# Kernel tuning notes

Hardware: AMD Instinct MI355X
Metric: run time of the kernel (lower is better)

## Reference

```python
import jax, jax.numpy as jnp
import numpy as np

N_POINTS = 1048576  # batch of evaluation points
HIDDEN = 128
N_HIDDEN_LAYERS = 9  # 128->128 layers between the input and output projections


def setup_inputs() -> dict:
    key = jax.random.key(0)
    ks = jax.random.split(key, 7)
    # Kaiming-ish scale so activations stay O(1) through the deep ReLU stack
    s_in = (2.0 / 4) ** 0.5
    s_h = (2.0 / HIDDEN) ** 0.5
    return {
        "x": jax.random.normal(ks[0], (N_POINTS, 4), dtype=jnp.float32),
        "W0": jax.random.normal(ks[1], (HIDDEN, 4), dtype=jnp.float32) * s_in,
        "b0": jnp.zeros((HIDDEN,), dtype=jnp.float32),
        "Wh": jax.random.normal(ks[2], (N_HIDDEN_LAYERS, HIDDEN, HIDDEN), dtype=jnp.float32) * s_h,
        "bh": jnp.zeros((N_HIDDEN_LAYERS, HIDDEN), dtype=jnp.float32),
        "Wout": jax.random.normal(ks[3], (1, HIDDEN), dtype=jnp.float32) * s_h,
        "bout": jnp.zeros((1,), dtype=jnp.float32),
    }


def reference(x, W0, b0, Wh, bh, Wout, bout):
    # Flatten: x is already [N, 4]; nn.Flatten collapses trailing dims to 4.
    h = jax.nn.relu(jnp.einsum("nd,hd->nh", x, W0) + b0)  # [N, 128]
    # 9 hidden Linear(128,128)+ReLU layers; small fixed layer loop (structural)
    for i in range(N_HIDDEN_LAYERS):
        h = jax.nn.relu(jnp.einsum("nh,oh->no", h, Wh[i]) + bh[i])
    logits = jnp.einsum("nh,oh->no", h, Wout) + bout  # [N, 1], no final ReLU
    return logits
```

## Files before the change

kernel.cpp:

```cpp
#include <hip/hip_runtime.h>
#include <stdint.h>

typedef _Float16 f16x8 __attribute__((ext_vector_type(8)));
typedef __fp16   fp16x2 __attribute__((ext_vector_type(2)));
typedef float    f32x16 __attribute__((ext_vector_type(16)));

union Frag {
  f16x8    v;
  uint32_t w[4];
  _Float16 h[8];
};

union CVec {
  float4 q[4];
  f32x16 v;
};

__device__ __forceinline__ uint32_t pack2h(float a, float b) {
  union { _Float16 h[2]; uint32_t u; } r;
  r.h[0] = (_Float16)a;
  r.h[1] = (_Float16)b;
  return r.u;
}

__device__ __forceinline__ uint32_t pkrtz(float a, float b) {
  union { fp16x2 h2; uint32_t u; } cv;
  cv.h2 = __builtin_amdgcn_cvt_pkrtz(a, b);
  return cv.u;
}

__device__ __forceinline__ void g2lds16(const void* g, void* l) {
  __builtin_amdgcn_global_load_lds(
      (const __attribute__((address_space(1))) uint32_t*)g,
      (__attribute__((address_space(3))) uint32_t*)l, 16, 0, 0);
}

__global__ void prep_kernel(const float* __restrict__ W0, const float* __restrict__ b0,
                            const float* __restrict__ Wh, const float* __restrict__ bh,
                            const float* __restrict__ Wout,
                            _Float16* __restrict__ wfrag, _Float16* __restrict__ w0frag,
                            float* __restrict__ biasC, _Float16* __restrict__ woutf16) {
  const int stride = gridDim.x * blockDim.x;
  for (int idx = blockIdx.x * blockDim.x + threadIdx.x; idx < 154880; idx += stride) {
    if (idx < 147456) {
      const int j = idx & 7, lane = (idx >> 3) & 63, kt = (idx >> 9) & 7,
                ot = (idx >> 12) & 3, l = idx >> 14;
      const int o = ot * 32 + (lane & 31);
      const int k = kt * 16 + (lane >> 5) * 8 + j;
      wfrag[idx] = (_Float16)Wh[(l * 128 + o) * 128 + k];
    } else if (idx < 147456 + 2048) {
      const int i = idx - 147456;
      const int j = i & 7, lane = (i >> 3) & 63, ot = i >> 9;
      const int o = ot * 32 + (lane & 31);
      const int k = (lane >> 5) * 8 + j;
      w0frag[i] = (_Float16)(k < 4 ? W0[o * 4 + k] : 0.0f);
    } else if (idx < 147456 + 2048 + 1280) {
      const int i = idx - (147456 + 2048);
      const int r = i & 15, hh = (i >> 4) & 1, ot = (i >> 5) & 3, l = i >> 7;
      const int row = (r & 3) + 8 * (r >> 2) + 4 * hh;
      const int o = ot * 32 + row;
      biasC[i] = (l == 0) ? b0[o] : bh[(l - 1) * 128 + o];
    } else {
      const int i = idx - (147456 + 2048 + 1280);
      const int j = i & 7, lane = (i >> 3) & 63, kt = i >> 9;
      const int k = kt * 16 + (lane >> 5) * 8 + j;
      woutf16[i] = ((lane & 31) == 0) ? (_Float16)Wout[k] : (_Float16)0.0f;
    }
  }
}

__global__ __launch_bounds__(256, 2) void mlp_fused(
    const float* __restrict__ x,
    const _Float16* __restrict__ wfrag,
    const _Float16* __restrict__ w0frag,
    const float* __restrict__ biasCg,
    const _Float16* __restrict__ woutf16,
    const float* __restrict__ boutp,
    float* __restrict__ out) {
  __shared__ __align__(16) unsigned char ldsW[2][32768];
  __shared__ __align__(16) float ldsBiasC[1280];

  const int t    = threadIdx.x;
  const int lane = t & 63;
  const int wv   = t >> 6;
  const int h    = lane >> 5;
  const int ln   = lane & 31;
  const long rowbase = (long)blockIdx.x * 256 + wv * 64;

  {
    const unsigned char* src = (const unsigned char*)wfrag;
#pragma unroll
    for (int i = 0; i < 8; ++i) {
      const int off = i * 4096 + t * 16;
      g2lds16(src + off, &ldsW[0][off]);
    }
    const unsigned char* bsrc = (const unsigned char*)biasCg;
    g2lds16(bsrc + t * 16, (unsigned char*)ldsBiasC + t * 16);
    if (t < 64) g2lds16(bsrc + (256 + t) * 16, (unsigned char*)ldsBiasC + (256 + t) * 16);
  }

  Frag   B[2][8];
  f32x16 acc[4][2];
  const f32x16 fzero = (f32x16)0.0f;

  auto load_cvec = [&](int l, int ot) -> f32x16 {
    CVec cv;
    const float* p = ldsBiasC + ((l * 4 + ot) * 2 + h) * 16;
#pragma unroll
    for (int g = 0; g < 4; ++g) cv.q[g] = *(const float4*)(p + g * 4);
    return cv.v;
  };

  Frag xb[2];
#pragma unroll
  for (int nt = 0; nt < 2; ++nt) {
    float4 xv = make_float4(0.f, 0.f, 0.f, 0.f);
    if (h == 0) xv = *(const float4*)(x + (rowbase + nt * 32 + ln) * 4);
    xb[nt].w[0] = pack2h(xv.x, xv.y);
    xb[nt].w[1] = pack2h(xv.z, xv.w);
    xb[nt].w[2] = 0u;
    xb[nt].w[3] = 0u;
  }

  __syncthreads();

#pragma unroll
  for (int ot = 0; ot < 4; ++ot) {
    const f16x8 a0 = *(const f16x8*)(w0frag + ot * 512 + lane * 8);
    const f32x16 cvec = load_cvec(0, ot);
    acc[ot][0] = __builtin_amdgcn_mfma_f32_32x32x16_f16(a0, xb[0].v, cvec, 0, 0, 0);
    acc[ot][1] = __builtin_amdgcn_mfma_f32_32x32x16_f16(a0, xb[1].v, cvec, 0, 0, 0);
  }

  auto do_epilogue = [&]() {
#pragma unroll
    for (int ot = 0; ot < 4; ++ot) {
#pragma unroll
      for (int nt = 0; nt < 2; ++nt) {
        uint32_t P[4][2];
#pragma unroll
        for (int g = 0; g < 4; ++g) {
#pragma unroll
          for (int c = 0; c < 2; ++c) {
            const uint32_t cv = pkrtz(acc[ot][nt][g * 4 + c * 2 + 0],
                                      acc[ot][nt][g * 4 + c * 2 + 1]);
            uint32_t r;
            asm("v_pk_max_f16 %0, %1, %2" : "=v"(r) : "v"(cv), "v"(0u));
            P[g][c] = r;
          }
        }
#pragma unroll
        for (int u = 0; u < 2; ++u) {
          uint32_t a0 = P[2 * u][0], b0v = P[2 * u + 1][0];
          uint32_t a1 = P[2 * u][1], b1v = P[2 * u + 1][1];
          asm("v_permlane32_swap_b32 %0, %1" : "+v"(a0), "+v"(b0v));
          asm("v_permlane32_swap_b32 %0, %1" : "+v"(a1), "+v"(b1v));
          Frag nb;
          nb.w[0] = a0;
          nb.w[1] = a1;
          nb.w[2] = b0v;
          nb.w[3] = b1v;
          B[nt][ot * 2 + u] = nb;
        }
      }
    }
  };

#pragma unroll
  for (int l = 1; l <= 9; ++l) {
    if (l < 9) {
      const unsigned char* src = (const unsigned char*)wfrag + (size_t)l * 32768;
#pragma unroll
      for (int i = 0; i < 8; ++i) {
        const int off = i * 4096 + t * 16;
        g2lds16(src + off, &ldsW[l & 1][off]);
      }
    }
    do_epilogue();
    const unsigned char* wl = &ldsW[(l - 1) & 1][0];
    __builtin_amdgcn_s_setprio(1);
#pragma unroll
    for (int kt = 0; kt < 8; ++kt) {
#pragma unroll
      for (int ot = 0; ot < 4; ++ot) {
        const f16x8 a = *(const f16x8*)(wl + ot * 8192 + kt * 1024 + lane * 16);
        if (kt == 0) {
          const f32x16 cvec = load_cvec(l, ot);
          acc[ot][0] = __builtin_amdgcn_mfma_f32_32x32x16_f16(a, B[0][kt].v, cvec, 0, 0, 0);
          acc[ot][1] = __builtin_amdgcn_mfma_f32_32x32x16_f16(a, B[1][kt].v, cvec, 0, 0, 0);
        } else {
          acc[ot][0] = __builtin_amdgcn_mfma_f32_32x32x16_f16(a, B[0][kt].v, acc[ot][0], 0, 0, 0);
          acc[ot][1] = __builtin_amdgcn_mfma_f32_32x32x16_f16(a, B[1][kt].v, acc[ot][1], 0, 0, 0);
        }
      }
    }
    __builtin_amdgcn_s_setprio(0);
    if (l < 9) __syncthreads();
  }

  {
    Frag wa[8];
#pragma unroll
    for (int kt = 0; kt < 8; ++kt)
      wa[kt].v = *(const f16x8*)(woutf16 + kt * 512 + lane * 8);
    const float boutv = *boutp;

    do_epilogue();

    f32x16 accO0 = fzero, accO1 = fzero;
#pragma unroll
    for (int kt = 0; kt < 8; ++kt) {
      accO0 = __builtin_amdgcn_mfma_f32_32x32x16_f16(wa[kt].v, B[0][kt].v, accO0, 0, 0, 0);
      accO1 = __builtin_amdgcn_mfma_f32_32x32x16_f16(wa[kt].v, B[1][kt].v, accO1, 0, 0, 0);
    }
    if (h == 0) {
      out[rowbase + ln]      = accO0[0] + boutv;
      out[rowbase + 32 + ln] = accO1[0] + boutv;
    }
  }
}

extern "C" void kernel_launch(void* const* d_in, const int* in_sizes, int n_in,
                              void* d_out, int out_size, void* d_ws, size_t ws_size,
                              hipStream_t stream) {
  (void)n_in; (void)out_size; (void)ws_size;
  const float* x    = (const float*)d_in[0];
  const float* W0   = (const float*)d_in[1];
  const float* b0   = (const float*)d_in[2];
  const float* Wh   = (const float*)d_in[3];
  const float* bh   = (const float*)d_in[4];
  const float* Wout = (const float*)d_in[5];
  const float* bout = (const float*)d_in[6];
  float* out = (float*)d_out;

  char* ws = (char*)d_ws;
  _Float16* wfrag   = (_Float16*)(ws);
  _Float16* w0frag  = (_Float16*)(ws + 294912);
  float*    biasC   = (float*)(ws + 299008);
  _Float16* woutf16 = (_Float16*)(ws + 304128);

  const int n = in_sizes[0] / 4;

  prep_kernel<<<dim3(160), dim3(256), 0, stream>>>(W0, b0, Wh, bh, Wout,
                                                   wfrag, w0frag, biasC, woutf16);
  mlp_fused<<<dim3(n / 256), dim3(256), 0, stream>>>(x, wfrag, w0frag, biasC,
                                                     woutf16, bout, out);
}
```

Measured before the change: 257.0 us.

## Halve rows per wave and double block threads to raise occupancy

Each wave now processes 32 rows instead of 64, and blocks grow to 512 threads covering the same 256 rows. Accumulator and activation-fragment registers per wave are halved, which allows more resident waves to hide the latency of the epilogue and MFMA chains. The cost is that each weight fragment loaded from LDS now feeds one MFMA instead of two, doubling LDS read traffic per row. Weight and bias staging loops are redistributed across the larger thread count.

```diff
diff --git a/kernel.cpp b/kernel.cpp
--- a/kernel.cpp
+++ b/kernel.cpp
@@ -69,7 +69,7 @@
   }
 }
 
-__global__ __launch_bounds__(256, 2) void mlp_fused(
+__global__ __launch_bounds__(512, 4) void mlp_fused(
     const float* __restrict__ x,
     const _Float16* __restrict__ wfrag,
     const _Float16* __restrict__ w0frag,
@@ -85,22 +85,23 @@
   const int wv   = t >> 6;
   const int h    = lane >> 5;
   const int ln   = lane & 31;
-  const long rowbase = (long)blockIdx.x * 256 + wv * 64;
+  const long rowbase = (long)blockIdx.x * 256 + wv * 32;
 
   {
     const unsigned char* src = (const unsigned char*)wfrag;
 #pragma unroll
-    for (int i = 0; i < 8; ++i) {
-      const int off = i * 4096 + t * 16;
+    for (int i = 0; i < 4; ++i) {
+      const int off = i * 8192 + t * 16;
       g2lds16(src + off, &ldsW[0][off]);
     }
-    const unsigned char* bsrc = (const unsigned char*)biasCg;
-    g2lds16(bsrc + t * 16, (unsigned char*)ldsBiasC + t * 16);
-    if (t < 64) g2lds16(bsrc + (256 + t) * 16, (unsigned char*)ldsBiasC + (256 + t) * 16);
-  }
-
-  Frag   B[2][8];
-  f32x16 acc[4][2];
+    if (t < 320) {
+      const unsigned char* bsrc = (const unsigned char*)biasCg;
+      g2lds16(bsrc + t * 16, (unsigned char*)ldsBiasC + t * 16);
+    }
+  }
+
+  Frag   B[8];
+  f32x16 acc[4];
   const f32x16 fzero = (f32x16)0.0f;
 
   auto load_cvec = [&](int l, int ot) -> f32x16 {
@@ -111,15 +112,42 @@
     return cv.v;
   };
 
-  Frag xb[2];
-#pragma unroll
-  for (int nt = 0; nt < 2; ++nt) {
+  auto e_chunk = [&](int ot) {
+    uint32_t P[4][2];
+#pragma unroll
+    for (int g = 0; g < 4; ++g) {
+#pragma unroll
+      for (int c = 0; c < 2; ++c) {
+        const uint32_t cv = pkrtz(acc[ot][g * 4 + c * 2 + 0],
+                                  acc[ot][g * 4 + c * 2 + 1]);
+        uint32_t r;
+        asm("v_pk_max_f16 %0, %1, %2" : "=v"(r) : "v"(cv), "v"(0u));
+        P[g][c] = r;
+      }
+    }
+#pragma unroll
+    for (int u = 0; u < 2; ++u) {
+      uint32_t a0 = P[2 * u][0], b0v = P[2 * u + 1][0];
+      uint32_t a1 = P[2 * u][1], b1v = P[2 * u + 1][1];
+      asm("v_permlane32_swap_b32 %0, %1" : "+v"(a0), "+v"(b0v));
+      asm("v_permlane32_swap_b32 %0, %1" : "+v"(a1), "+v"(b1v));
+      Frag nb;
+      nb.w[0] = a0;
+      nb.w[1] = a1;
+      nb.w[2] = b0v;
+      nb.w[3] = b1v;
+      B[ot * 2 + u] = nb;
+    }
+  };
+
+  Frag xb;
+  {
     float4 xv = make_float4(0.f, 0.f, 0.f, 0.f);
-    if (h == 0) xv = *(const float4*)(x + (rowbase + nt * 32 + ln) * 4);
-    xb[nt].w[0] = pack2h(xv.x, xv.y);
-    xb[nt].w[1] = pack2h(xv.z, xv.w);
-    xb[nt].w[2] = 0u;
-    xb[nt].w[3] = 0u;
+    if (h == 0) xv = *(const float4*)(x + (rowbase + ln) * 4);
+    xb.w[0] = pack2h(xv.x, xv.y);
+    xb.w[1] = pack2h(xv.z, xv.w);
+    xb.w[2] = 0u;
+    xb.w[3] = 0u;
   }
 
   __syncthreads();
@@ -128,55 +156,21 @@
   for (int ot = 0; ot < 4; ++ot) {
     const f16x8 a0 = *(const f16x8*)(w0frag + ot * 512 + lane * 8);
     const f32x16 cvec = load_cvec(0, ot);
-    acc[ot][0] = __builtin_amdgcn_mfma_f32_32x32x16_f16(a0, xb[0].v, cvec, 0, 0, 0);
-    acc[ot][1] = __builtin_amdgcn_mfma_f32_32x32x16_f16(a0, xb[1].v, cvec, 0, 0, 0);
-  }
-
-  auto do_epilogue = [&]() {
-#pragma unroll
-    for (int ot = 0; ot < 4; ++ot) {
-#pragma unroll
-      for (int nt = 0; nt < 2; ++nt) {
-        uint32_t P[4][2];
-#pragma unroll
-        for (int g = 0; g < 4; ++g) {
-#pragma unroll
-          for (int c = 0; c < 2; ++c) {
-            const uint32_t cv = pkrtz(acc[ot][nt][g * 4 + c * 2 + 0],
-                                      acc[ot][nt][g * 4 + c * 2 + 1]);
-            uint32_t r;
-            asm("v_pk_max_f16 %0, %1, %2" : "=v"(r) : "v"(cv), "v"(0u));
-            P[g][c] = r;
-          }
-        }
-#pragma unroll
-        for (int u = 0; u < 2; ++u) {
-          uint32_t a0 = P[2 * u][0], b0v = P[2 * u + 1][0];
-          uint32_t a1 = P[2 * u][1], b1v = P[2 * u + 1][1];
-          asm("v_permlane32_swap_b32 %0, %1" : "+v"(a0), "+v"(b0v));
-          asm("v_permlane32_swap_b32 %0, %1" : "+v"(a1), "+v"(b1v));
-          Frag nb;
-          nb.w[0] = a0;
-          nb.w[1] = a1;
-          nb.w[2] = b0v;
-          nb.w[3] = b1v;
-          B[nt][ot * 2 + u] = nb;
-        }
-      }
-    }
-  };
+    acc[ot] = __builtin_amdgcn_mfma_f32_32x32x16_f16(a0, xb.v, cvec, 0, 0, 0);
+  }
 
 #pragma unroll
   for (int l = 1; l <= 9; ++l) {
     if (l < 9) {
       const unsigned char* src = (const unsigned char*)wfrag + (size_t)l * 32768;
 #pragma unroll
-      for (int i = 0; i < 8; ++i) {
-        const int off = i * 4096 + t * 16;
+      for (int i = 0; i < 4; ++i) {
+        const int off = i * 8192 + t * 16;
         g2lds16(src + off, &ldsW[l & 1][off]);
       }
     }
-    do_epilogue();
+#pragma unroll
+    for (int c = 0; c < 4; ++c) e_chunk(c);
     const unsigned char* wl = &ldsW[(l - 1) & 1][0];
     __builtin_amdgcn_s_setprio(1);
 #pragma unroll
@@ -186,11 +180,9 @@
         const f16x8 a = *(const f16x8*)(wl + ot * 8192 + kt * 1024 + lane * 16);
         if (kt == 0) {
           const f32x16 cvec = load_cvec(l, ot);
-          acc[ot][0] = __builtin_amdgcn_mfma_f32_32x32x16_f16(a, B[0][kt].v, cvec, 0, 0, 0);
-          acc[ot][1] = __builtin_amdgcn_mfma_f32_32x32x16_f16(a, B[1][kt].v, cvec, 0, 0, 0);
+          acc[ot] = __builtin_amdgcn_mfma_f32_32x32x16_f16(a, B[0].v, cvec, 0, 0, 0);
         } else {
-          acc[ot][0] = __builtin_amdgcn_mfma_f32_32x32x16_f16(a, B[0][kt].v, acc[ot][0], 0, 0, 0);
-          acc[ot][1] = __builtin_amdgcn_mfma_f32_32x32x16_f16(a, B[1][kt].v, acc[ot][1], 0, 0, 0);
+          acc[ot] = __builtin_amdgcn_mfma_f32_32x32x16_f16(a, B[kt].v, acc[ot], 0, 0, 0);
         }
       }
     }
@@ -205,18 +197,14 @@
       wa[kt].v = *(const f16x8*)(woutf16 + kt * 512 + lane * 8);
     const float boutv = *boutp;
 
-    do_epilogue();
-
-    f32x16 accO0 = fzero, accO1 = fzero;
-#pragma unroll
-    for (int kt = 0; kt < 8; ++kt) {
-      accO0 = __builtin_amdgcn_mfma_f32_32x32x16_f16(wa[kt].v, B[0][kt].v, accO0, 0, 0, 0);
-      accO1 = __builtin_amdgcn_mfma_f32_32x32x16_f16(wa[kt].v, B[1][kt].v, accO1, 0, 0, 0);
-    }
-    if (h == 0) {
-      out[rowbase + ln]      = accO0[0] + boutv;
-      out[rowbase + 32 + ln] = accO1[0] + boutv;
-    }
+#pragma unroll
+    for (int c = 0; c < 4; ++c) e_chunk(c);
+
+    f32x16 accO = fzero;
+#pragma unroll
+    for (int kt = 0; kt < 8; ++kt)
+      accO = __builtin_amdgcn_mfma_f32_32x32x16_f16(wa[kt].v, B[kt].v, accO, 0, 0, 0);
+    if (h == 0) out[rowbase + ln] = accO[0] + boutv;
   }
 }
 
@@ -243,6 +231,6 @@
 
   prep_kernel<<<dim3(160), dim3(256), 0, stream>>>(W0, b0, Wh, bh, Wout,
                                                    wfrag, w0frag, biasC, woutf16);
-  mlp_fused<<<dim3(n / 256), dim3(256), 0, stream>>>(x, wfrag, w0frag, biasC,
+  mlp_fused<<<dim3(n / 256), dim3(512), 0, stream>>>(x, wfrag, w0frag, biasC,
                                                      woutf16, bout, out);
 }
```

After: 269.3 us. 1.05x slower.
